# Kernel tuning notes

Hardware: AMD Instinct MI355X
Metric: run time of the kernel (lower is better)

The kernel has to match this reference:

```python
import jax, jax.numpy as jnp
import numpy as np

W = 256  # attention_window, must match init_kwargs


def _gather_band(full, w):
    # full: [..., w, 3w]; returns band[..., w, 2w+1] with band[r, j] = full[r, r + j]
    *lead, x, three_w = full.shape
    flat = full.reshape(*lead, x * three_w)
    flat = jnp.pad(flat, [(0, 0)] * len(lead) + [(0, x)])  # len -> x*(3w+1)
    return flat.reshape(*lead, x, three_w + 1)[..., : 2 * w + 1]


def _scatter_band(band, w):
    # band: [..., w, 2w+1]; returns full[..., w, 3w] with full[r, r + j] = band[r, j], 0 elsewhere
    *lead, x, win = band.shape
    padded = jnp.pad(band, [(0, 0)] * len(lead) + [(0, 0), (0, x)])  # width 3w+1
    flat = padded.reshape(*lead, x * (win + x))
    return flat[..., : x * (win + x - 1)].reshape(*lead, x, win + x - 1)


def _windows(x_pad, nc, w):
    # x_pad: [BH, (nc+2)*w, D] -> overlapping windows [BH, nc, 3w, D] (stride w)
    BH, _, D = x_pad.shape
    xr = x_pad.reshape(BH, nc + 2, w, D)
    return jnp.concatenate([xr[:, :-2], xr[:, 1:-1], xr[:, 2:]], axis=2)


def _longformer(q, k, v, w):
    B, H, S, D = q.shape
    BH = B * H
    nc = S // w
    q2 = q.reshape(BH, S, D)
    k2 = k.reshape(BH, S, D)
    v2 = v.reshape(BH, S, D)
    # banded QK via overlapping chunks: each chunk of w queries sees 3w keys
    qc = q2.reshape(BH, nc, w, D)
    kp = jnp.pad(k2, ((0, 0), (w, w), (0, 0)))
    kw = _windows(kp, nc, w)  # [BH, nc, 3w, D]
    full = jnp.einsum('bcxd,bcyd->bcxy', qc, kw) / jnp.sqrt(jnp.float32(D))
    band = _gather_band(full, w).reshape(BH, S, 2 * w + 1)
    # mask window positions that fall outside [0, S) (== mask_start_end_extra_local_tokens)
    key_idx = jnp.arange(S)[:, None] - w + jnp.arange(2 * w + 1)[None, :]
    invalid = (key_idx < 0) | (key_idx >= S)
    band = jnp.where(invalid[None], -jnp.inf, band)
    attn_probs = jax.nn.softmax(band.astype(jnp.float32), axis=-1)  # [BH, S, 2w+1]
    # banded PV: scatter probs into [w, 3w] per chunk, matmul against 3w value windows
    pb = _scatter_band(attn_probs.reshape(BH, nc, w, 2 * w + 1), w)  # [BH, nc, w, 3w]
    vp = jnp.pad(v2, ((0, 0), (w, w), (0, 0)))
    vw = _windows(vp, nc, w)  # [BH, nc, 3w, D]
    context = jnp.einsum('bcxy,bcyd->bcxd', pb, vw).reshape(B, H, S, D)
    return context, attn_probs


def setup_inputs() -> dict:
    key = jax.random.key(0)
    kq, kk, kv = jax.random.split(key, 3)
    shape = (2, 16, 4096, 64)
    return {
        'q': jax.random.normal(kq, shape, dtype=jnp.float32),
        'k': jax.random.normal(kk, shape, dtype=jnp.float32),
        'v': jax.random.normal(kv, shape, dtype=jnp.float32),
        'numeric_embedding_manager': 0,  # unused by forward
    }


def reference(q, k, v, numeric_embedding_manager):
    return _longformer(q, k, v, W)
```

## Files before the change

kernel.cpp:

```cpp
#include <hip/hip_runtime.h>
#include <math.h>

#define S_LEN 4096
#define HDIM  64
#define WTOK  256
#define WIN   513
#define NBH   32

static constexpr size_t CTX_ELEMS = (size_t)NBH * S_LEN * HDIM;

__global__ __launch_bounds__(256) void qk_softmax_probs(
    const float* __restrict__ q, const float* __restrict__ k,
    float* __restrict__ probs)
{
    __shared__ float qs[64 * HDIM];

    const int bid  = blockIdx.x;
    const int bh   = bid >> 6;
    const int q0   = (bid & 63) << 6;
    const int tid  = threadIdx.x;
    const int lane = tid & 63;
    const int wave = tid >> 6;

    const size_t bh_base = (size_t)bh * S_LEN * HDIM;

    {
        const float4* src = reinterpret_cast<const float4*>(q + bh_base + (size_t)q0 * HDIM);
        float4* dst = reinterpret_cast<float4*>(qs);
        #pragma unroll
        for (int i = 0; i < 4; ++i) dst[tid + 256 * i] = src[tid + 256 * i];
    }
    __syncthreads();

    const float4* kbh4 = reinterpret_cast<const float4*>(k + bh_base);

    const int qr0 = q0 + wave * 16;

    const float4* kp[9];
    bool kok[9];
    #pragma unroll
    for (int t = 0; t < 9; ++t) {
        int key = qr0 - WTOK + t * 64 + lane;
        kok[t] = (key >= 0) && (key < S_LEN);
        int kc  = min(max(key, 0), S_LEN - 1);
        kp[t] = kbh4 + (size_t)kc * 16;
    }

    float acc[16][9];
    #pragma unroll
    for (int rr = 0; rr < 16; ++rr)
        #pragma unroll
        for (int t = 0; t < 9; ++t) acc[rr][t] = 0.0f;

    const float4* qrow = reinterpret_cast<const float4*>(qs + (wave * 16) * HDIM);

    for (int d4 = 0; d4 < 16; ++d4) {
        float4 kv[9];
        #pragma unroll
        for (int t = 0; t < 9; ++t) kv[t] = kp[t][d4];
        #pragma unroll
        for (int rr = 0; rr < 16; ++rr) {
            float4 qv = qrow[rr * 16 + d4];
            #pragma unroll
            for (int t = 0; t < 9; ++t) {
                acc[rr][t] = fmaf(qv.x, kv[t].x, acc[rr][t]);
                acc[rr][t] = fmaf(qv.y, kv[t].y, acc[rr][t]);
                acc[rr][t] = fmaf(qv.z, kv[t].z, acc[rr][t]);
                acc[rr][t] = fmaf(qv.w, kv[t].w, acc[rr][t]);
            }
        }
    }

    const float scale = 0.125f;

    #pragma unroll
    for (int rr = 0; rr < 16; ++rr) {
        float s[9];
        float m = -INFINITY;
        #pragma unroll
        for (int t = 0; t < 9; ++t) {
            int j = t * 64 + lane - rr;
            bool ok = kok[t] && (j >= 0) && (j <= 2 * WTOK);
            s[t] = ok ? acc[rr][t] * scale : -INFINITY;
            m = fmaxf(m, s[t]);
        }
        #pragma unroll
        for (int off = 32; off > 0; off >>= 1)
            m = fmaxf(m, __shfl_xor(m, off, 64));

        float z = 0.0f;
        #pragma unroll
        for (int t = 0; t < 9; ++t) {
            s[t] = __expf(s[t] - m);
            z += s[t];
        }
        #pragma unroll
        for (int off = 32; off > 0; off >>= 1)
            z += __shfl_xor(z, off, 64);
        float inv = 1.0f / z;

        size_t base = ((size_t)bh * S_LEN + (qr0 + rr)) * WIN;
        #pragma unroll
        for (int t = 0; t < 9; ++t) {
            int j = t * 64 + lane - rr;
            if (j >= 0 && j <= 2 * WTOK)
                probs[base + j] = s[t] * inv;
        }
    }
}

__global__ __launch_bounds__(256) void pv_banded(
    const float* __restrict__ probs, const float* __restrict__ v,
    float* __restrict__ ctx)
{
    __shared__ float pt[4][32 * 64];

    const int bid  = blockIdx.x;
    const int bh   = bid >> 4;
    const int tid  = threadIdx.x;
    const int lane = tid & 63;
    const int w    = tid >> 6;
    const int R0   = (bid & 15) * 256 + w * 64;
    const int rb   = lane >> 3;
    const int db   = lane & 7;

    const float4* v4  = reinterpret_cast<const float4*>(v + (size_t)bh * S_LEN * HDIM);
    float*        ptw = pt[w];
    const float4* pt4 = reinterpret_cast<const float4*>(ptw);

    const int row_mine = R0 + lane;
    const float* prow = probs + ((size_t)bh * S_LEN + row_mine) * WIN;

    float acc[8][8];
    #pragma unroll
    for (int i = 0; i < 8; ++i)
        #pragma unroll
        for (int j = 0; j < 8; ++j) acc[i][j] = 0.0f;

    for (int t = 0; t < 18; ++t) {
        const int kb = R0 - WTOK + t * 32;

        const int j0 = kb - row_mine + WTOK;
        #pragma unroll
        for (int c = 0; c < 32; ++c) {
            int j = j0 + c;
            float pv = (j >= 0 && j <= 2 * WTOK) ? prow[j] : 0.0f;
            ptw[c * 64 + lane] = pv;
        }
        __builtin_amdgcn_wave_barrier();

        #pragma unroll
        for (int kk = 0; kk < 32; ++kk) {
            int kc = min(max(kb + kk, 0), S_LEN - 1);
            const float4* vr = v4 + (size_t)kc * 16;
            float4 b0 = vr[db * 2];
            float4 b1 = vr[db * 2 + 1];
            float4 a0 = pt4[kk * 16 + rb * 2];
            float4 a1 = pt4[kk * 16 + rb * 2 + 1];
            float a[8] = {a0.x, a0.y, a0.z, a0.w, a1.x, a1.y, a1.z, a1.w};
            float b[8] = {b0.x, b0.y, b0.z, b0.w, b1.x, b1.y, b1.z, b1.w};
            #pragma unroll
            for (int ri = 0; ri < 8; ++ri)
                #pragma unroll
                for (int ci = 0; ci < 8; ++ci)
                    acc[ri][ci] = fmaf(a[ri], b[ci], acc[ri][ci]);
        }
        __builtin_amdgcn_wave_barrier();
    }

    float* cbh = ctx + (size_t)bh * S_LEN * HDIM;
    #pragma unroll
    for (int ri = 0; ri < 8; ++ri) {
        int row = R0 + rb * 8 + ri;
        float4 o0 = make_float4(acc[ri][0], acc[ri][1], acc[ri][2], acc[ri][3]);
        float4 o1 = make_float4(acc[ri][4], acc[ri][5], acc[ri][6], acc[ri][7]);
        float4* out4 = reinterpret_cast<float4*>(cbh + (size_t)row * HDIM + db * 8);
        out4[0] = o0;
        out4[1] = o1;
    }
}

extern "C" void kernel_launch(void* const* d_in, const int* in_sizes, int n_in,
                              void* d_out, int out_size, void* d_ws, size_t ws_size,
                              hipStream_t stream)
{
    const float* q = (const float*)d_in[0];
    const float* k = (const float*)d_in[1];
    const float* v = (const float*)d_in[2];
    (void)in_sizes; (void)n_in; (void)d_ws; (void)ws_size; (void)out_size;

    float* ctx   = (float*)d_out;
    float* probs = (float*)d_out + CTX_ELEMS;

    hipLaunchKernelGGL(qk_softmax_probs, dim3(NBH * 64), dim3(256), 0, stream,
                       q, k, probs);
    hipLaunchKernelGGL(pv_banded, dim3(NBH * 16), dim3(256), 0, stream,
                       probs, v, ctx);
}
```

Before: 1.145 ms.

## Retile QK kernel and make PV stage probability tiles cooperatively with register prefetch

The QK/softmax kernel now gives each block 32 query rows instead of 64, so each wave owns 8 rows. This halves the accumulator registers and doubles the grid, with launch bounds asking for 4 blocks per CU. The PV kernel is restructured so the whole block loads a 64x64 probability tile with coalesced float4 reads. It exploits the band layout (row stride 513 gives an address of r*512 + k + W) and keeps a padded shared tile, prefetching the next tile into registers while computing the current one. Each thread now computes a 2x8 output tile instead of 8x8, which raises the number of V loads per FMA. Edge rows can also read slightly past the probs rows; those values are masked, but the reads may touch memory outside the buffer.

```diff
diff --git a/kernel.cpp b/kernel.cpp
--- a/kernel.cpp
+++ b/kernel.cpp
@@ -9,15 +9,15 @@
 
 static constexpr size_t CTX_ELEMS = (size_t)NBH * S_LEN * HDIM;
 
-__global__ __launch_bounds__(256) void qk_softmax_probs(
+__global__ __launch_bounds__(256, 4) void qk_softmax_probs(
     const float* __restrict__ q, const float* __restrict__ k,
     float* __restrict__ probs)
 {
-    __shared__ float qs[64 * HDIM];
+    __shared__ float qs[32 * HDIM];
 
     const int bid  = blockIdx.x;
-    const int bh   = bid >> 6;
-    const int q0   = (bid & 63) << 6;
+    const int bh   = bid >> 7;
+    const int q0   = (bid & 127) << 5;
     const int tid  = threadIdx.x;
     const int lane = tid & 63;
     const int wave = tid >> 6;
@@ -27,46 +27,45 @@
     {
         const float4* src = reinterpret_cast<const float4*>(q + bh_base + (size_t)q0 * HDIM);
         float4* dst = reinterpret_cast<float4*>(qs);
-        #pragma unroll
-        for (int i = 0; i < 4; ++i) dst[tid + 256 * i] = src[tid + 256 * i];
+        dst[tid]       = src[tid];
+        dst[tid + 256] = src[tid + 256];
     }
     __syncthreads();
 
-    const float4* kbh4 = reinterpret_cast<const float4*>(k + bh_base);
-
-    const int qr0 = q0 + wave * 16;
-
-    const float4* kp[9];
-    bool kok[9];
+    const int qr0     = q0 + wave * 8;
+    const int keybase = qr0 - WTOK + lane;
+    const char* kbase = reinterpret_cast<const char*>(k + bh_base);
+
+    int koff[9];
     #pragma unroll
     for (int t = 0; t < 9; ++t) {
-        int key = qr0 - WTOK + t * 64 + lane;
-        kok[t] = (key >= 0) && (key < S_LEN);
-        int kc  = min(max(key, 0), S_LEN - 1);
-        kp[t] = kbh4 + (size_t)kc * 16;
-    }
-
-    float acc[16][9];
-    #pragma unroll
-    for (int rr = 0; rr < 16; ++rr)
+        int kc = min(max(keybase + t * 64, 0), S_LEN - 1);
+        koff[t] = kc << 8;
+    }
+
+    float acc[8][9];
+    #pragma unroll
+    for (int rr = 0; rr < 8; ++rr)
         #pragma unroll
         for (int t = 0; t < 9; ++t) acc[rr][t] = 0.0f;
 
-    const float4* qrow = reinterpret_cast<const float4*>(qs + (wave * 16) * HDIM);
-
+    const int qrow0 = wave * 8;
+
+    #pragma unroll 4
     for (int d4 = 0; d4 < 16; ++d4) {
-        float4 kv[9];
-        #pragma unroll
-        for (int t = 0; t < 9; ++t) kv[t] = kp[t][d4];
-        #pragma unroll
-        for (int rr = 0; rr < 16; ++rr) {
-            float4 qv = qrow[rr * 16 + d4];
+        float4 qv[8];
+        #pragma unroll
+        for (int rr = 0; rr < 8; ++rr)
+            qv[rr] = *reinterpret_cast<const float4*>(&qs[(qrow0 + rr) * HDIM + d4 * 4]);
+        #pragma unroll
+        for (int t = 0; t < 9; ++t) {
+            float4 kv = *reinterpret_cast<const float4*>(kbase + koff[t] + d4 * 16);
             #pragma unroll
-            for (int t = 0; t < 9; ++t) {
-                acc[rr][t] = fmaf(qv.x, kv[t].x, acc[rr][t]);
-                acc[rr][t] = fmaf(qv.y, kv[t].y, acc[rr][t]);
-                acc[rr][t] = fmaf(qv.z, kv[t].z, acc[rr][t]);
-                acc[rr][t] = fmaf(qv.w, kv[t].w, acc[rr][t]);
+            for (int rr = 0; rr < 8; ++rr) {
+                acc[rr][t] = fmaf(qv[rr].x, kv.x, acc[rr][t]);
+                acc[rr][t] = fmaf(qv[rr].y, kv.y, acc[rr][t]);
+                acc[rr][t] = fmaf(qv[rr].z, kv.z, acc[rr][t]);
+                acc[rr][t] = fmaf(qv[rr].w, kv.w, acc[rr][t]);
             }
         }
     }
@@ -74,13 +73,14 @@
     const float scale = 0.125f;
 
     #pragma unroll
-    for (int rr = 0; rr < 16; ++rr) {
+    for (int rr = 0; rr < 8; ++rr) {
         float s[9];
         float m = -INFINITY;
         #pragma unroll
         for (int t = 0; t < 9; ++t) {
-            int j = t * 64 + lane - rr;
-            bool ok = kok[t] && (j >= 0) && (j <= 2 * WTOK);
+            int key = keybase + t * 64;
+            int j   = t * 64 + lane - rr;
+            bool ok = (key >= 0) && (key < S_LEN) && (j >= 0) && (j <= 2 * WTOK);
             s[t] = ok ? acc[rr][t] * scale : -INFINITY;
             m = fmaxf(m, s[t]);
         }
@@ -109,74 +109,110 @@
     }
 }
 
-__global__ __launch_bounds__(256) void pv_banded(
+__global__ __launch_bounds__(256, 4) void pv_banded(
     const float* __restrict__ probs, const float* __restrict__ v,
     float* __restrict__ ctx)
 {
-    __shared__ float pt[4][32 * 64];
+    __shared__ float pt[64 * 65];
 
     const int bid  = blockIdx.x;
-    const int bh   = bid >> 4;
+    const int bh   = bid >> 6;
+    const int R    = (bid & 63) << 6;
     const int tid  = threadIdx.x;
     const int lane = tid & 63;
     const int w    = tid >> 6;
-    const int R0   = (bid & 15) * 256 + w * 64;
     const int rb   = lane >> 3;
     const int db   = lane & 7;
-
-    const float4* v4  = reinterpret_cast<const float4*>(v + (size_t)bh * S_LEN * HDIM);
-    float*        ptw = pt[w];
-    const float4* pt4 = reinterpret_cast<const float4*>(ptw);
-
-    const int row_mine = R0 + lane;
-    const float* prow = probs + ((size_t)bh * S_LEN + row_mine) * WIN;
-
-    float acc[8][8];
-    #pragma unroll
-    for (int i = 0; i < 8; ++i)
+    const int rloc0 = w * 16 + rb * 2;
+
+    const size_t pbase = (size_t)bh * S_LEN * WIN;
+    const float4* v4 = reinterpret_cast<const float4*>(v + (size_t)bh * S_LEN * HDIM);
+
+    const int ri0 = tid >> 4;
+    const int c0  = (tid & 15) << 2;
+
+    float4 stg[4];
+
+    auto stage_load = [&](int t) {
+        const int K0 = R - WTOK + (t << 6);
+        #pragma unroll
+        for (int s = 0; s < 4; ++s) {
+            int ri = ri0 + (s << 4);
+            int r  = R + ri;
+            const float* p = probs + pbase + (size_t)r * 512 + (K0 + WTOK) + c0;
+            float4 val = *reinterpret_cast<const float4*>(p);
+            int k0 = K0 + c0;
+            val.x = (k0     >= r - WTOK && k0     <= r + WTOK) ? val.x : 0.0f;
+            val.y = (k0 + 1 >= r - WTOK && k0 + 1 <= r + WTOK) ? val.y : 0.0f;
+            val.z = (k0 + 2 >= r - WTOK && k0 + 2 <= r + WTOK) ? val.z : 0.0f;
+            val.w = (k0 + 3 >= r - WTOK && k0 + 3 <= r + WTOK) ? val.w : 0.0f;
+            stg[s] = val;
+        }
+    };
+    auto stage_write = [&]() {
+        #pragma unroll
+        for (int s = 0; s < 4; ++s) {
+            int ri = ri0 + (s << 4);
+            float* d = &pt[ri * 65 + c0];
+            d[0] = stg[s].x; d[1] = stg[s].y; d[2] = stg[s].z; d[3] = stg[s].w;
+        }
+    };
+
+    float acc[2][8];
+    #pragma unroll
+    for (int i = 0; i < 2; ++i)
         #pragma unroll
         for (int j = 0; j < 8; ++j) acc[i][j] = 0.0f;
 
-    for (int t = 0; t < 18; ++t) {
-        const int kb = R0 - WTOK + t * 32;
-
-        const int j0 = kb - row_mine + WTOK;
-        #pragma unroll
-        for (int c = 0; c < 32; ++c) {
-            int j = j0 + c;
-            float pv = (j >= 0 && j <= 2 * WTOK) ? prow[j] : 0.0f;
-            ptw[c * 64 + lane] = pv;
-        }
-        __builtin_amdgcn_wave_barrier();
-
-        #pragma unroll
-        for (int kk = 0; kk < 32; ++kk) {
-            int kc = min(max(kb + kk, 0), S_LEN - 1);
+    stage_load(0);
+    stage_write();
+    __syncthreads();
+
+    for (int t = 0; t < 9; ++t) {
+        if (t < 8) stage_load(t + 1);
+        const int K0 = R - WTOK + (t << 6);
+
+        #pragma unroll 8
+        for (int kk = 0; kk < 64; ++kk) {
+            int kc = min(max(K0 + kk, 0), S_LEN - 1);
             const float4* vr = v4 + (size_t)kc * 16;
             float4 b0 = vr[db * 2];
             float4 b1 = vr[db * 2 + 1];
-            float4 a0 = pt4[kk * 16 + rb * 2];
-            float4 a1 = pt4[kk * 16 + rb * 2 + 1];
-            float a[8] = {a0.x, a0.y, a0.z, a0.w, a1.x, a1.y, a1.z, a1.w};
-            float b[8] = {b0.x, b0.y, b0.z, b0.w, b1.x, b1.y, b1.z, b1.w};
-            #pragma unroll
-            for (int ri = 0; ri < 8; ++ri)
-                #pragma unroll
-                for (int ci = 0; ci < 8; ++ci)
-                    acc[ri][ci] = fmaf(a[ri], b[ci], acc[ri][ci]);
-        }
-        __builtin_amdgcn_wave_barrier();
-    }
-
-    float* cbh = ctx + (size_t)bh * S_LEN * HDIM;
-    #pragma unroll
-    for (int ri = 0; ri < 8; ++ri) {
-        int row = R0 + rb * 8 + ri;
-        float4 o0 = make_float4(acc[ri][0], acc[ri][1], acc[ri][2], acc[ri][3]);
-        float4 o1 = make_float4(acc[ri][4], acc[ri][5], acc[ri][6], acc[ri][7]);
-        float4* out4 = reinterpret_cast<float4*>(cbh + (size_t)row * HDIM + db * 8);
-        out4[0] = o0;
-        out4[1] = o1;
+            float p0 = pt[rloc0 * 65 + kk];
+            float p1 = pt[(rloc0 + 1) * 65 + kk];
+            acc[0][0] = fmaf(p0, b0.x, acc[0][0]);
+            acc[0][1] = fmaf(p0, b0.y, acc[0][1]);
+            acc[0][2] = fmaf(p0, b0.z, acc[0][2]);
+            acc[0][3] = fmaf(p0, b0.w, acc[0][3]);
+            acc[0][4] = fmaf(p0, b1.x, acc[0][4]);
+            acc[0][5] = fmaf(p0, b1.y, acc[0][5]);
+            acc[0][6] = fmaf(p0, b1.z, acc[0][6]);
+            acc[0][7] = fmaf(p0, b1.w, acc[0][7]);
+            acc[1][0] = fmaf(p1, b0.x, acc[1][0]);
+            acc[1][1] = fmaf(p1, b0.y, acc[1][1]);
+            acc[1][2] = fmaf(p1, b0.z, acc[1][2]);
+            acc[1][3] = fmaf(p1, b0.w, acc[1][3]);
+            acc[1][4] = fmaf(p1, b1.x, acc[1][4]);
+            acc[1][5] = fmaf(p1, b1.y, acc[1][5]);
+            acc[1][6] = fmaf(p1, b1.z, acc[1][6]);
+            acc[1][7] = fmaf(p1, b1.w, acc[1][7]);
+        }
+        __syncthreads();
+        if (t < 8) {
+            stage_write();
+            __syncthreads();
+        }
+    }
+
+    float* cb = ctx + (size_t)bh * S_LEN * HDIM;
+    #pragma unroll
+    for (int rr = 0; rr < 2; ++rr) {
+        int r = R + rloc0 + rr;
+        float4 o0 = make_float4(acc[rr][0], acc[rr][1], acc[rr][2], acc[rr][3]);
+        float4 o1 = make_float4(acc[rr][4], acc[rr][5], acc[rr][6], acc[rr][7]);
+        float4* o = reinterpret_cast<float4*>(cb + (size_t)r * HDIM + db * 8);
+        o[0] = o0;
+        o[1] = o1;
     }
 }
 
@@ -192,8 +228,8 @@
     float* ctx   = (float*)d_out;
     float* probs = (float*)d_out + CTX_ELEMS;
 
-    hipLaunchKernelGGL(qk_softmax_probs, dim3(NBH * 64), dim3(256), 0, stream,
+    hipLaunchKernelGGL(qk_softmax_probs, dim3(NBH * 128), dim3(256), 0, stream,
                        q, k, probs);
-    hipLaunchKernelGGL(pv_banded, dim3(NBH * 16), dim3(256), 0, stream,
+    hipLaunchKernelGGL(pv_banded, dim3(NBH * 64), dim3(256), 0, stream,
                        probs, v, ctx);
 }
```

New measurement: 3.167 ms. 2.77x slower.
